# Kernel optimization log

Measured on AMD Instinct MI355X. Metric: run time of the kernel, lower is better.

Reference implementation:

```python
import jax, jax.numpy as jnp
import numpy as np

N_NODES = 50000
IN_CH = 128
HID_CH = 128   # 2 * out_channels
OUT_CH = 64
N_EDGES = 800000


def setup_inputs() -> dict:
    key = jax.random.key(0)
    k1, k2, k3, k4 = jax.random.split(key, 4)
    x = jax.random.normal(k1, (N_NODES, IN_CH), dtype=jnp.float32)
    edge_index = jax.random.randint(k2, (2, N_EDGES), 0, N_NODES, dtype=jnp.int64)
    # Glorot-ish init for weights
    W1 = jax.random.normal(k3, (IN_CH, HID_CH), dtype=jnp.float32) * (1.0 / np.sqrt(IN_CH))
    b1 = jnp.zeros((HID_CH,), dtype=jnp.float32)
    W2 = jax.random.normal(k4, (HID_CH, OUT_CH), dtype=jnp.float32) * (1.0 / np.sqrt(HID_CH))
    b2 = jnp.zeros((OUT_CH,), dtype=jnp.float32)
    return {"x": x, "edge_index": edge_index, "W1": W1, "b1": b1, "W2": W2, "b2": b2}


def _gcn_norm(edge_index, num_nodes):
    """Add self-loops and compute symmetric normalization coeffs (PyG GCNConv default)."""
    loops = jnp.arange(num_nodes, dtype=edge_index.dtype)
    src = jnp.concatenate([edge_index[0], loops])  # [E + N]
    dst = jnp.concatenate([edge_index[1], loops])
    ones = jnp.ones_like(dst, dtype=jnp.float32)
    deg = jax.ops.segment_sum(ones, dst, num_segments=num_nodes)  # in-degree incl self-loop
    dinv = jnp.where(deg > 0, jax.lax.rsqrt(deg), 0.0)
    norm = dinv[src] * dinv[dst]  # [E + N]
    return src, dst, norm


def _gcn_conv(x, src, dst, norm, W, b, num_nodes):
    h = x @ W                                        # dense transform [N, d_out]
    msg = h[src] * norm[:, None]                     # gather + scale  [E+N, d_out]
    out = jax.ops.segment_sum(msg, dst, num_segments=num_nodes)  # scatter-add
    return out + b


def reference(x, edge_index, W1, b1, W2, b2):
    n = x.shape[0]
    src, dst, norm = _gcn_norm(edge_index, n)
    h = _gcn_conv(x, src, dst, norm, W1, b1, n)
    h = jax.nn.relu(h)
    out = _gcn_conv(h, src, dst, norm, W2, b2, n)
    return out
```

## Files before the change

### kernel.cpp

```cpp
#include <hip/hip_runtime.h>
#include <hip/hip_fp16.h>
#include <math.h>

#define IN_CH 128
#define CAP 64


template <int NOUT, bool IN_HALF, bool SCALE>
__device__ __forceinline__ void gemm_tile(
    const void* __restrict__ Av, const float* __restrict__ W,
    const int* __restrict__ deg, __half* __restrict__ G,
    int row0, int M, float* As, float* Bs) {
    constexpr int KC = 32;
    constexpr int AP = KC + 4;
    constexpr int TCG = NOUT / 8;
    constexpr int BST = KC * 8 + 4;
    constexpr int TM = 64 / (256 / TCG);
    int tid = threadIdx.x;
    int cgi = tid % TCG;
    int rg = tid / TCG;
    int r0 = rg * TM;

    float acc[TM][8];
#pragma unroll
    for (int r = 0; r < TM; ++r)
#pragma unroll
        for (int c = 0; c < 8; ++c) acc[r][c] = 0.f;

    for (int kc0 = 0; kc0 < IN_CH; kc0 += KC) {
        __syncthreads();
        if constexpr (IN_HALF) {
            const __half* Ah = (const __half*)Av;
            int r = tid >> 2;
            int grp = tid & 3;
            float f[8];
            if (row0 + r < M) {
                uint4 raw = *(const uint4*)(Ah + (size_t)(row0 + r) * IN_CH + kc0 + grp * 8);
                const __half2* h2 = (const __half2*)&raw;
#pragma unroll
                for (int q = 0; q < 4; ++q) {
                    float2 fv = __half22float2(h2[q]);
                    f[2 * q] = fv.x;
                    f[2 * q + 1] = fv.y;
                }
            } else {
#pragma unroll
                for (int q = 0; q < 8; ++q) f[q] = 0.f;
            }
            *(float4*)(As + r * AP + grp * 8) = make_float4(f[0], f[1], f[2], f[3]);
            *(float4*)(As + r * AP + grp * 8 + 4) = make_float4(f[4], f[5], f[6], f[7]);
        } else {
            const float* Af = (const float*)Av;
            for (int idx = tid; idx < 64 * (KC / 4); idx += 256) {
                int r = idx >> 3;
                int c4 = (idx & 7) * 4;
                float4 v = make_float4(0.f, 0.f, 0.f, 0.f);
                if (row0 + r < M) v = *(const float4*)(Af + (size_t)(row0 + r) * IN_CH + kc0 + c4);
                *(float4*)(As + r * AP + c4) = v;
            }
        }
        for (int idx = tid; idx < KC * (NOUT / 4); idx += 256) {
            int kk = idx / (NOUT / 4);
            int col = (idx % (NOUT / 4)) * 4;
            int cgw = col >> 3;
            int j = col & 7;
            *(float4*)(Bs + cgw * BST + kk * 8 + j) = *(const float4*)(W + (size_t)(kc0 + kk) * NOUT + col);
        }
        __syncthreads();

        for (int k = 0; k < KC; k += 4) {
            float4 a4[TM];
#pragma unroll
            for (int r = 0; r < TM; ++r) a4[r] = *(const float4*)(As + (r0 + r) * AP + k);
#pragma unroll
            for (int kk = 0; kk < 4; ++kk) {
                float4 b0 = *(const float4*)(Bs + cgi * BST + (k + kk) * 8);
                float4 b1 = *(const float4*)(Bs + cgi * BST + (k + kk) * 8 + 4);
#pragma unroll
                for (int r = 0; r < TM; ++r) {
                    float a = (kk == 0) ? a4[r].x : (kk == 1) ? a4[r].y : (kk == 2) ? a4[r].z : a4[r].w;
                    acc[r][0] += a * b0.x;
                    acc[r][1] += a * b0.y;
                    acc[r][2] += a * b0.z;
                    acc[r][3] += a * b0.w;
                    acc[r][4] += a * b1.x;
                    acc[r][5] += a * b1.y;
                    acc[r][6] += a * b1.z;
                    acc[r][7] += a * b1.w;
                }
            }
        }
    }

#pragma unroll
    for (int r = 0; r < TM; ++r) {
        int row = row0 + r0 + r;
        if (row < M) {
            float d = 1.f;
            if constexpr (SCALE) d = rsqrtf((float)(deg[row] + 1));
            union { __half2 h[4]; uint4 u; } cv;
            cv.h[0] = __floats2half2_rn(d * acc[r][0], d * acc[r][1]);
            cv.h[1] = __floats2half2_rn(d * acc[r][2], d * acc[r][3]);
            cv.h[2] = __floats2half2_rn(d * acc[r][4], d * acc[r][5]);
            cv.h[3] = __floats2half2_rn(d * acc[r][6], d * acc[r][7]);
            *(uint4*)(G + (size_t)row * NOUT + cgi * 8) = cv.u;
        }
    }
}


__global__ __launch_bounds__(256, 4) void k_p1(const float* __restrict__ x, const float* __restrict__ W1,
                                               __half* __restrict__ g1, const int* __restrict__ src,
                                               const int* __restrict__ dst, int* __restrict__ deg,
                                               unsigned short* __restrict__ slot, int N, int E, int GB) {
    __shared__ float As[64 * 36];
    __shared__ float Bs[16 * 260];
    int gtid = blockIdx.x * 256 + threadIdx.x;
    int gsz = gridDim.x * 256;
    for (int e = gtid; e < E; e += gsz) {
        int d = dst[e];
        int s = src[e];
        int r = atomicAdd(&deg[d], 1);
        if (r < CAP) slot[(size_t)d * CAP + r] = (unsigned short)s;
    }
    for (int t = blockIdx.x; t < GB; t += gridDim.x)
        gemm_tile<128, false, false>(x, W1, deg, g1, t * 64, N, As, Bs);
}

__global__ __launch_bounds__(256) void k_p2(const __half* __restrict__ g, const int* __restrict__ deg,
                                            const unsigned short* __restrict__ slot,
                                            const float* __restrict__ b1, __half* __restrict__ a1, int N) {
    int i = blockIdx.x * 4 + (threadIdx.x >> 6);
    if (i >= N) return;
    int lane = threadIdx.x & 63;
    const __half2* gp = (const __half2*)g;
    int degi = deg[i];
    int m = min(degi, CAP);
    float dinv_i = rsqrtf((float)(degi + 1));
    float2 self = __half22float2(gp[(size_t)i * 64 + lane]);
    float2 acc = make_float2(dinv_i * self.x, dinv_i * self.y);
    const unsigned short* sl = slot + (size_t)i * CAP;
    int r = 0;
    for (; r + 8 <= m; r += 8) {
        union { uint4 u; unsigned short us[8]; } iv;
        iv.u = *(const uint4*)(sl + r);
        int s[8];
#pragma unroll
        for (int j = 0; j < 8; ++j) s[j] = iv.us[j];
        __half2 v[8];
#pragma unroll
        for (int j = 0; j < 8; ++j) v[j] = gp[(size_t)s[j] * 64 + lane];
        float ds[8];
#pragma unroll
        for (int j = 0; j < 8; ++j) ds[j] = rsqrtf((float)(deg[s[j]] + 1));
#pragma unroll
        for (int j = 0; j < 8; ++j) {
            float2 f = __half22float2(v[j]);
            acc.x += ds[j] * f.x;
            acc.y += ds[j] * f.y;
        }
    }
    for (; r < m; ++r) {
        int s = sl[r];
        float dsv = rsqrtf((float)(deg[s] + 1));
        float2 f = __half22float2(gp[(size_t)s * 64 + lane]);
        acc.x += dsv * f.x;
        acc.y += dsv * f.y;
    }
    float2 b = ((const float2*)b1)[lane];
    float ox = fmaxf(dinv_i * acc.x + b.x, 0.f);
    float oy = fmaxf(dinv_i * acc.y + b.y, 0.f);
    ((__half2*)a1)[(size_t)i * 64 + lane] = __floats2half2_rn(ox, oy);
}

__global__ __launch_bounds__(256, 4) void k_p3(const __half* __restrict__ a1, const float* __restrict__ W2,
                                               const int* __restrict__ deg, __half* __restrict__ g2,
                                               int N, int GB) {
    __shared__ float As[64 * 36];
    __shared__ float Bs[16 * 260];
    for (int t = blockIdx.x; t < GB; t += gridDim.x)
        gemm_tile<64, true, true>(a1, W2, deg, g2, t * 64, N, As, Bs);
}

__global__ __launch_bounds__(256) void k_p4(const __half* __restrict__ g2, const int* __restrict__ deg,
                                            const unsigned short* __restrict__ slot,
                                            const float* __restrict__ b2, float* __restrict__ out, int N) {
    int i = blockIdx.x * 4 + (threadIdx.x >> 6);
    if (i >= N) return;
    int lane = threadIdx.x & 63;
    int degi = deg[i];
    int m = min(degi, CAP);
    float dinv_i = rsqrtf((float)(degi + 1));
    float acc = __half2float(g2[(size_t)i * 64 + lane]);
    const unsigned short* sl = slot + (size_t)i * CAP;
    int r = 0;
    for (; r + 8 <= m; r += 8) {
        union { uint4 u; unsigned short us[8]; } iv;
        iv.u = *(const uint4*)(sl + r);
        int s[8];
#pragma unroll
        for (int j = 0; j < 8; ++j) s[j] = iv.us[j];
        __half v[8];
#pragma unroll
        for (int j = 0; j < 8; ++j) v[j] = g2[(size_t)s[j] * 64 + lane];
#pragma unroll
        for (int j = 0; j < 8; ++j) acc += __half2float(v[j]);
    }
    for (; r < m; ++r) acc += __half2float(g2[(size_t)sl[r] * 64 + lane]);
    out[(size_t)i * 64 + lane] = dinv_i * acc + b2[lane];
}


static inline size_t align256(size_t v) { return (v + 255) & ~(size_t)255; }

extern "C" void kernel_launch(void* const* d_in, const int* in_sizes, int n_in,
                              void* d_out, int out_size, void* d_ws, size_t ws_size,
                              hipStream_t stream) {
    const float* x = (const float*)d_in[0];
    const int* ei = (const int*)d_in[1];
    const float* W1 = (const float*)d_in[2];
    const float* b1 = (const float*)d_in[3];
    const float* W2 = (const float*)d_in[4];
    const float* b2 = (const float*)d_in[5];
    float* out = (float*)d_out;

    int N = in_sizes[0] / IN_CH;
    int E = in_sizes[1] / 2;
    const int* src = ei;
    const int* dst = ei + E;

    char* p = (char*)d_ws;
    int* deg = (int*)p;                        p += align256((size_t)N * 4);
    unsigned short* slot = (unsigned short*)p; p += align256((size_t)N * CAP * 2);
    __half* g1 = (__half*)p;                   p += align256((size_t)N * 128 * 2);
    __half* a1 = (__half*)p;                   p += align256((size_t)N * 128 * 2);

    int GB = (N + 63) / 64;

    hipMemsetAsync(deg, 0, (size_t)N * 4, stream);
    k_p1<<<1568, 256, 0, stream>>>(x, W1, g1, src, dst, deg, slot, N, E, GB);
    k_p2<<<(N + 3) / 4, 256, 0, stream>>>(g1, deg, slot, b1, a1, N);
    k_p3<<<GB, 256, 0, stream>>>(a1, W2, deg, g1, N, GB);
    k_p4<<<(N + 3) / 4, 256, 0, stream>>>(g1, deg, slot, b2, out, N);
}
```

Measured before the change: 232.5 us.

## Fuse layer-1 aggregation with layer-2 GEMM and split p1 blocks by role

The layer-1 gather/aggregate, bias and ReLU are fused with the layer-2 dense transform in one kernel. The activated rows stay in shared memory as fp32, so the a1 intermediate is never written to or read back from global memory, and one kernel launch is removed. In k_p1, dedicated blocks now do either a GEMM tile or edge bucketing, instead of every block running a grid-stride edge loop and then its GEMM tiles. The fused kernel has only GB (about 782) blocks of 256 threads with larger shared memory, so the latency-bound gather runs with less parallelism than the old per-node kernel.

Result: slower. 290.8 us (+25.1%).

```diff
diff --git a/kernel.cpp b/kernel.cpp
--- a/kernel.cpp
+++ b/kernel.cpp
@@ -6,17 +6,35 @@
 #define CAP 64
 
 
-template <int NOUT, bool IN_HALF, bool SCALE>
-__device__ __forceinline__ void gemm_tile(
-    const void* __restrict__ Av, const float* __restrict__ W,
-    const int* __restrict__ deg, __half* __restrict__ G,
-    int row0, int M, float* As, float* Bs) {
+__global__ __launch_bounds__(256, 4) void k_p1(const float* __restrict__ x, const float* __restrict__ W1,
+                                               __half* __restrict__ g1, const int* __restrict__ src,
+                                               const int* __restrict__ dst, int* __restrict__ deg,
+                                               unsigned short* __restrict__ slot, int N, int E, int GB) {
     constexpr int KC = 32;
     constexpr int AP = KC + 4;
-    constexpr int TCG = NOUT / 8;
+    constexpr int TCG = 16;
     constexpr int BST = KC * 8 + 4;
-    constexpr int TM = 64 / (256 / TCG);
+    constexpr int TM = 4;
+    __shared__ float As[64 * AP];
+    __shared__ float Bs[TCG * BST];
     int tid = threadIdx.x;
+
+    if ((int)blockIdx.x >= GB) {
+        int base = ((int)blockIdx.x - GB) * 1024;
+#pragma unroll
+        for (int k = 0; k < 4; ++k) {
+            int e = base + k * 256 + tid;
+            if (e < E) {
+                int d = dst[e];
+                int s = src[e];
+                int r = atomicAdd(&deg[d], 1);
+                if (r < CAP) slot[(size_t)d * CAP + r] = (unsigned short)s;
+            }
+        }
+        return;
+    }
+
+    int row0 = blockIdx.x * 64;
     int cgi = tid % TCG;
     int rg = tid / TCG;
     int r0 = rg * TM;
@@ -28,43 +46,20 @@
         for (int c = 0; c < 8; ++c) acc[r][c] = 0.f;
 
     for (int kc0 = 0; kc0 < IN_CH; kc0 += KC) {
-        __syncthreads();
-        if constexpr (IN_HALF) {
-            const __half* Ah = (const __half*)Av;
-            int r = tid >> 2;
-            int grp = tid & 3;
-            float f[8];
-            if (row0 + r < M) {
-                uint4 raw = *(const uint4*)(Ah + (size_t)(row0 + r) * IN_CH + kc0 + grp * 8);
-                const __half2* h2 = (const __half2*)&raw;
-#pragma unroll
-                for (int q = 0; q < 4; ++q) {
-                    float2 fv = __half22float2(h2[q]);
-                    f[2 * q] = fv.x;
-                    f[2 * q + 1] = fv.y;
-                }
-            } else {
-#pragma unroll
-                for (int q = 0; q < 8; ++q) f[q] = 0.f;
-            }
-            *(float4*)(As + r * AP + grp * 8) = make_float4(f[0], f[1], f[2], f[3]);
-            *(float4*)(As + r * AP + grp * 8 + 4) = make_float4(f[4], f[5], f[6], f[7]);
-        } else {
-            const float* Af = (const float*)Av;
-            for (int idx = tid; idx < 64 * (KC / 4); idx += 256) {
-                int r = idx >> 3;
-                int c4 = (idx & 7) * 4;
-                float4 v = make_float4(0.f, 0.f, 0.f, 0.f);
-                if (row0 + r < M) v = *(const float4*)(Af + (size_t)(row0 + r) * IN_CH + kc0 + c4);
-                *(float4*)(As + r * AP + c4) = v;
-            }
-        }
-        for (int idx = tid; idx < KC * (NOUT / 4); idx += 256) {
-            int kk = idx / (NOUT / 4);
-            int col = (idx % (NOUT / 4)) * 4;
+        if (kc0 > 0) __syncthreads();
+        for (int idx = tid; idx < 64 * (KC / 4); idx += 256) {
+            int r = idx >> 3;
+            int c4 = (idx & 7) * 4;
+            float4 v = make_float4(0.f, 0.f, 0.f, 0.f);
+            if (row0 + r < N) v = *(const float4*)(x + (size_t)(row0 + r) * IN_CH + kc0 + c4);
+            *(float4*)(As + r * AP + c4) = v;
+        }
+        for (int idx = tid; idx < KC * (128 / 4); idx += 256) {
+            int kk = idx / 32;
+            int col = (idx % 32) * 4;
             int cgw = col >> 3;
             int j = col & 7;
-            *(float4*)(Bs + cgw * BST + kk * 8 + j) = *(const float4*)(W + (size_t)(kc0 + kk) * NOUT + col);
+            *(float4*)(Bs + cgw * BST + kk * 8 + j) = *(const float4*)(W1 + (size_t)(kc0 + kk) * 128 + col);
         }
         __syncthreads();
 
@@ -95,92 +90,135 @@
 #pragma unroll
     for (int r = 0; r < TM; ++r) {
         int row = row0 + r0 + r;
-        if (row < M) {
-            float d = 1.f;
-            if constexpr (SCALE) d = rsqrtf((float)(deg[row] + 1));
+        if (row < N) {
             union { __half2 h[4]; uint4 u; } cv;
-            cv.h[0] = __floats2half2_rn(d * acc[r][0], d * acc[r][1]);
-            cv.h[1] = __floats2half2_rn(d * acc[r][2], d * acc[r][3]);
-            cv.h[2] = __floats2half2_rn(d * acc[r][4], d * acc[r][5]);
-            cv.h[3] = __floats2half2_rn(d * acc[r][6], d * acc[r][7]);
-            *(uint4*)(G + (size_t)row * NOUT + cgi * 8) = cv.u;
-        }
-    }
-}
-
-
-__global__ __launch_bounds__(256, 4) void k_p1(const float* __restrict__ x, const float* __restrict__ W1,
-                                               __half* __restrict__ g1, const int* __restrict__ src,
-                                               const int* __restrict__ dst, int* __restrict__ deg,
-                                               unsigned short* __restrict__ slot, int N, int E, int GB) {
-    __shared__ float As[64 * 36];
-    __shared__ float Bs[16 * 260];
-    int gtid = blockIdx.x * 256 + threadIdx.x;
-    int gsz = gridDim.x * 256;
-    for (int e = gtid; e < E; e += gsz) {
-        int d = dst[e];
-        int s = src[e];
-        int r = atomicAdd(&deg[d], 1);
-        if (r < CAP) slot[(size_t)d * CAP + r] = (unsigned short)s;
-    }
-    for (int t = blockIdx.x; t < GB; t += gridDim.x)
-        gemm_tile<128, false, false>(x, W1, deg, g1, t * 64, N, As, Bs);
-}
-
-__global__ __launch_bounds__(256) void k_p2(const __half* __restrict__ g, const int* __restrict__ deg,
-                                            const unsigned short* __restrict__ slot,
-                                            const float* __restrict__ b1, __half* __restrict__ a1, int N) {
-    int i = blockIdx.x * 4 + (threadIdx.x >> 6);
-    if (i >= N) return;
-    int lane = threadIdx.x & 63;
-    const __half2* gp = (const __half2*)g;
-    int degi = deg[i];
-    int m = min(degi, CAP);
-    float dinv_i = rsqrtf((float)(degi + 1));
-    float2 self = __half22float2(gp[(size_t)i * 64 + lane]);
-    float2 acc = make_float2(dinv_i * self.x, dinv_i * self.y);
-    const unsigned short* sl = slot + (size_t)i * CAP;
-    int r = 0;
-    for (; r + 8 <= m; r += 8) {
-        union { uint4 u; unsigned short us[8]; } iv;
-        iv.u = *(const uint4*)(sl + r);
-        int s[8];
-#pragma unroll
-        for (int j = 0; j < 8; ++j) s[j] = iv.us[j];
-        __half2 v[8];
-#pragma unroll
-        for (int j = 0; j < 8; ++j) v[j] = gp[(size_t)s[j] * 64 + lane];
-        float ds[8];
-#pragma unroll
-        for (int j = 0; j < 8; ++j) ds[j] = rsqrtf((float)(deg[s[j]] + 1));
-#pragma unroll
-        for (int j = 0; j < 8; ++j) {
-            float2 f = __half22float2(v[j]);
-            acc.x += ds[j] * f.x;
-            acc.y += ds[j] * f.y;
-        }
-    }
-    for (; r < m; ++r) {
-        int s = sl[r];
-        float dsv = rsqrtf((float)(deg[s] + 1));
-        float2 f = __half22float2(gp[(size_t)s * 64 + lane]);
-        acc.x += dsv * f.x;
-        acc.y += dsv * f.y;
-    }
-    float2 b = ((const float2*)b1)[lane];
-    float ox = fmaxf(dinv_i * acc.x + b.x, 0.f);
-    float oy = fmaxf(dinv_i * acc.y + b.y, 0.f);
-    ((__half2*)a1)[(size_t)i * 64 + lane] = __floats2half2_rn(ox, oy);
-}
-
-__global__ __launch_bounds__(256, 4) void k_p3(const __half* __restrict__ a1, const float* __restrict__ W2,
-                                               const int* __restrict__ deg, __half* __restrict__ g2,
-                                               int N, int GB) {
-    __shared__ float As[64 * 36];
-    __shared__ float Bs[16 * 260];
-    for (int t = blockIdx.x; t < GB; t += gridDim.x)
-        gemm_tile<64, true, true>(a1, W2, deg, g2, t * 64, N, As, Bs);
-}
+            cv.h[0] = __floats2half2_rn(acc[r][0], acc[r][1]);
+            cv.h[1] = __floats2half2_rn(acc[r][2], acc[r][3]);
+            cv.h[2] = __floats2half2_rn(acc[r][4], acc[r][5]);
+            cv.h[3] = __floats2half2_rn(acc[r][6], acc[r][7]);
+            *(uint4*)(g1 + (size_t)row * 128 + cgi * 8) = cv.u;
+        }
+    }
+}
+
+
+__global__ __launch_bounds__(256, 2) void k_q2(const __half* __restrict__ g1, const int* __restrict__ deg,
+                                               const unsigned short* __restrict__ slot,
+                                               const float* __restrict__ b1, const float* __restrict__ W2,
+                                               __half* __restrict__ g2, int N) {
+    constexpr int AP = 132;
+    constexpr int BST = 128 * 8 + 4;
+    __shared__ float As[64 * AP];
+    __shared__ float Bs[8 * BST];
+    int tid = threadIdx.x;
+    int row0 = blockIdx.x * 64;
+
+    for (int idx = tid; idx < 128 * (64 / 4); idx += 256) {
+        int kk = idx / 16;
+        int col = (idx % 16) * 4;
+        int cgw = col >> 3;
+        int j = col & 7;
+        *(float4*)(Bs + cgw * BST + kk * 8 + j) = *(const float4*)(W2 + (size_t)kk * 64 + col);
+    }
+
+    {
+        int wv = tid >> 6, lane = tid & 63;
+        const __half2* gp = (const __half2*)g1;
+        float2 b = ((const float2*)b1)[lane];
+        for (int j16 = 0; j16 < 16; ++j16) {
+            int i = row0 + wv * 16 + j16;
+            if (i >= N) break;
+            int degi = deg[i];
+            int m = min(degi, CAP);
+            float dinv_i = rsqrtf((float)(degi + 1));
+            float2 self = __half22float2(gp[(size_t)i * 64 + lane]);
+            float2 acc = make_float2(dinv_i * self.x, dinv_i * self.y);
+            const unsigned short* sl = slot + (size_t)i * CAP;
+            int r = 0;
+            for (; r + 8 <= m; r += 8) {
+                union { uint4 u; unsigned short us[8]; } iv;
+                iv.u = *(const uint4*)(sl + r);
+                int s[8];
+#pragma unroll
+                for (int j = 0; j < 8; ++j) s[j] = iv.us[j];
+                __half2 v[8];
+#pragma unroll
+                for (int j = 0; j < 8; ++j) v[j] = gp[(size_t)s[j] * 64 + lane];
+                float ds[8];
+#pragma unroll
+                for (int j = 0; j < 8; ++j) ds[j] = rsqrtf((float)(deg[s[j]] + 1));
+#pragma unroll
+                for (int j = 0; j < 8; ++j) {
+                    float2 f = __half22float2(v[j]);
+                    acc.x += ds[j] * f.x;
+                    acc.y += ds[j] * f.y;
+                }
+            }
+            for (; r < m; ++r) {
+                int s = sl[r];
+                float dsv = rsqrtf((float)(deg[s] + 1));
+                float2 f = __half22float2(gp[(size_t)s * 64 + lane]);
+                acc.x += dsv * f.x;
+                acc.y += dsv * f.y;
+            }
+            float ox = fmaxf(dinv_i * acc.x + b.x, 0.f);
+            float oy = fmaxf(dinv_i * acc.y + b.y, 0.f);
+            int rr = wv * 16 + j16;
+            As[rr * AP + 2 * lane] = ox;
+            As[rr * AP + 2 * lane + 1] = oy;
+        }
+    }
+    __syncthreads();
+
+    {
+        int cgi = tid % 8;
+        int rg = tid / 8;
+        int r0 = rg * 2;
+        float acc[2][8];
+#pragma unroll
+        for (int r = 0; r < 2; ++r)
+#pragma unroll
+            for (int c = 0; c < 8; ++c) acc[r][c] = 0.f;
+
+        for (int k = 0; k < 128; k += 4) {
+            float4 a4[2];
+#pragma unroll
+            for (int r = 0; r < 2; ++r) a4[r] = *(const float4*)(As + (r0 + r) * AP + k);
+#pragma unroll
+            for (int kk = 0; kk < 4; ++kk) {
+                float4 b0 = *(const float4*)(Bs + cgi * BST + (k + kk) * 8);
+                float4 b1v = *(const float4*)(Bs + cgi * BST + (k + kk) * 8 + 4);
+#pragma unroll
+                for (int r = 0; r < 2; ++r) {
+                    float a = (kk == 0) ? a4[r].x : (kk == 1) ? a4[r].y : (kk == 2) ? a4[r].z : a4[r].w;
+                    acc[r][0] += a * b0.x;
+                    acc[r][1] += a * b0.y;
+                    acc[r][2] += a * b0.z;
+                    acc[r][3] += a * b0.w;
+                    acc[r][4] += a * b1v.x;
+                    acc[r][5] += a * b1v.y;
+                    acc[r][6] += a * b1v.z;
+                    acc[r][7] += a * b1v.w;
+                }
+            }
+        }
+
+#pragma unroll
+        for (int r = 0; r < 2; ++r) {
+            int row = row0 + r0 + r;
+            if (row < N) {
+                float d = rsqrtf((float)(deg[row] + 1));
+                union { __half2 h[4]; uint4 u; } cv;
+                cv.h[0] = __floats2half2_rn(d * acc[r][0], d * acc[r][1]);
+                cv.h[1] = __floats2half2_rn(d * acc[r][2], d * acc[r][3]);
+                cv.h[2] = __floats2half2_rn(d * acc[r][4], d * acc[r][5]);
+                cv.h[3] = __floats2half2_rn(d * acc[r][6], d * acc[r][7]);
+                *(uint4*)(g2 + (size_t)row * 64 + cgi * 8) = cv.u;
+            }
+        }
+    }
+}
+
 
 __global__ __launch_bounds__(256) void k_p4(const __half* __restrict__ g2, const int* __restrict__ deg,
                                             const unsigned short* __restrict__ slot,
@@ -233,13 +271,13 @@
     int* deg = (int*)p;                        p += align256((size_t)N * 4);
     unsigned short* slot = (unsigned short*)p; p += align256((size_t)N * CAP * 2);
     __half* g1 = (__half*)p;                   p += align256((size_t)N * 128 * 2);
-    __half* a1 = (__half*)p;                   p += align256((size_t)N * 128 * 2);
+    __half* g2 = (__half*)p;                   p += align256((size_t)N * 64 * 2);
 
     int GB = (N + 63) / 64;
+    int BB = (E + 1023) / 1024;
 
     hipMemsetAsync(deg, 0, (size_t)N * 4, stream);
-    k_p1<<<1568, 256, 0, stream>>>(x, W1, g1, src, dst, deg, slot, N, E, GB);
-    k_p2<<<(N + 3) / 4, 256, 0, stream>>>(g1, deg, slot, b1, a1, N);
-    k_p3<<<GB, 256, 0, stream>>>(a1, W2, deg, g1, N, GB);
-    k_p4<<<(N + 3) / 4, 256, 0, stream>>>(g1, deg, slot, b2, out, N);
-}
+    k_p1<<<GB + BB, 256, 0, stream>>>(x, W1, g1, src, dst, deg, slot, N, E, GB);
+    k_q2<<<GB, 256, 0, stream>>>(g1, deg, slot, b1, W2, g2, N);
+    k_p4<<<(N + 3) / 4, 256, 0, stream>>>(g2, deg, slot, b2, out, N);
+}
```
